# Optimization experiments

Measured on AMD Instinct MI355X. Metric: run time of the kernel, lower is better.

Reference implementation:

```python
import jax, jax.numpy as jnp
import numpy as np

NUM_HEADS = 8


def _nearest_idx(x, x_grid):
    # x: [b,n,dx]; x_grid: [b,H,W,dx] regular grid -> flat nearest cell index [b,n]
    b = x.shape[0]
    H, W = x_grid.shape[1], x_grid.shape[2]
    gf = x_grid.reshape(b, H * W, -1)
    lo = gf[:, :1]   # min corner [b,1,dx]
    hi = gf[:, -1:]  # max corner [b,1,dx]
    dims = jnp.asarray([H, W], dtype=x.dtype)
    t = (x - lo) / (hi - lo) * (dims - 1.0)
    idx = jnp.clip(jnp.round(t), 0.0, dims - 1.0).astype(jnp.int32)  # [b,n,2]
    return idx[..., 0] * W + idx[..., 1]


def _cumcount(idx):
    # per-batch cumulative count of each value, in order of appearance
    b, n = idx.shape
    order = jnp.argsort(idx, axis=1, stable=True)
    s = jnp.take_along_axis(idx, order, axis=1)
    ar = jnp.arange(n)
    new_run = jnp.concatenate([jnp.ones((b, 1), bool), s[:, 1:] != s[:, :-1]], axis=1)
    run_start = jax.lax.cummax(jnp.where(new_run, ar, 0), axis=1)
    cc_sorted = (ar - run_start).astype(jnp.int32)
    return jnp.zeros((b, n), jnp.int32).at[jnp.arange(b)[:, None], order].set(cc_sorted)


def _mhca(q_in, kv, mask, Wq, Wk, Wv, Wo):
    # q_in: [B,1,e]; kv: [B,K,e]; mask: [B,K] (True = attend)
    B, K, e = kv.shape
    dh = e // NUM_HEADS
    q = (q_in @ Wq).reshape(B, 1, NUM_HEADS, dh)
    k = (kv @ Wk).reshape(B, K, NUM_HEADS, dh)
    v = (kv @ Wv).reshape(B, K, NUM_HEADS, dh)
    scores = jnp.einsum('bqhd,bkhd->bhqk', q, k) / jnp.sqrt(jnp.asarray(dh, q.dtype))
    scores = jnp.where(mask[:, None, None, :], scores, jnp.finfo(scores.dtype).min)
    attn = jax.nn.softmax(scores, axis=-1)
    out = jnp.einsum('bhqk,bkhd->bqhd', attn, v).reshape(B, 1, e)
    return out @ Wo


def setup_inputs() -> dict:
    key = jax.random.key(0)
    ks = jax.random.split(key, 8)
    b, n, e, H, W = 8, 8192, 128, 64, 64
    x = jax.random.uniform(ks[0], (b, n, 2), jnp.float32)
    z = jax.random.normal(ks[1], (b, n, e), jnp.float32)
    g0 = jnp.linspace(0.0, 1.0, H)
    g1 = jnp.linspace(0.0, 1.0, W)
    mg = jnp.stack(jnp.meshgrid(g0, g1, indexing='ij'), axis=-1)  # [H,W,2]
    x_grid = jnp.broadcast_to(mg, (b, H, W, 2)).astype(jnp.float32)
    z_grid = jax.random.normal(ks[2], (b, H, W, e), jnp.float32)
    latent = jax.random.normal(ks[3], (e,), jnp.float32)
    scale = 1.0 / np.sqrt(e).astype(np.float32)
    Wq = jax.random.normal(ks[4], (e, e), jnp.float32) * scale
    Wk = jax.random.normal(ks[5], (e, e), jnp.float32) * scale
    Wv = jax.random.normal(ks[6], (e, e), jnp.float32) * scale
    Wo = jax.random.normal(ks[7], (e, e), jnp.float32) * scale
    return {"x": x, "z": z, "x_grid": x_grid, "z_grid": z_grid, "latent": latent,
            "Wq": Wq, "Wk": Wk, "Wv": Wv, "Wo": Wo, "max_patch": 20}


def reference(x, z, x_grid, z_grid, latent, Wq, Wk, Wv, Wo, max_patch):
    b, n, e = z.shape
    H, W = x_grid.shape[1], x_grid.shape[2]
    S = H * W
    nearest = _nearest_idx(x, x_grid)                    # [b,n]
    cc = _cumcount(nearest)                              # [b,n]
    bidx = jnp.broadcast_to(jnp.arange(b)[:, None], (b, n))
    valid = cc < max_patch
    slot = jnp.where(valid, cc, 0)
    # ragged scatter: pack each point's z into its grid cell's padded sequence
    joint = jnp.zeros((b, S, max_patch, e), z.dtype)
    joint = joint.at[bidx, nearest, slot].add(z * valid[..., None].astype(z.dtype))
    zg_flat = z_grid.reshape(b, S, e)
    joint = jnp.concatenate([joint, zg_flat[:, :, None, :]], axis=2)  # [b,S,P+1,e]
    counts = jnp.zeros((b, S), jnp.int32).at[bidx, nearest].add(1)
    mask = jnp.arange(max_patch + 1)[None, None, :] < jnp.minimum(counts, max_patch)[..., None]
    mask = mask.at[..., -1].set(True)  # grid token always attended
    joint = joint.reshape(b * S, max_patch + 1, e)
    mask = mask.reshape(b * S, max_patch + 1)
    q = jnp.broadcast_to(latent, (b * S, 1, e))          # z0_grid queries
    zg = _mhca(q, joint, mask, Wq, Wk, Wv, Wo)           # [b*S,1,e]
    zg = zg.reshape(b, H, W, e)
    return x_grid, zg
```

## Files before the change

kernel.cpp:

```cpp
#include <hip/hip_runtime.h>
#include <hip/hip_bf16.h>
#include <cstdint>
#include <cstddef>

#define S_CELLS 4096
#define NB      8
#define NPTS    8192
#define E       128
#define MAXP    20
#define NHEADS  8
#define NPT_ROWS (NB * NPTS)
#define NGR_ROWS (NB * S_CELLS)
#define NTOK     (NPT_ROWS + NGR_ROWS)


typedef __attribute__((ext_vector_type(8))) short bf16x8;
typedef __attribute__((ext_vector_type(4))) float f32x4;

__device__ __forceinline__ unsigned short f2bf_bits(float f) {
    unsigned u = __float_as_uint(f);
    unsigned rounded = u + 0x7FFFu + ((u >> 16) & 1u);
    return (unsigned short)(rounded >> 16);
}
__device__ __forceinline__ float bf2f(unsigned short u) {
    return __uint_as_float(((unsigned)u) << 16);
}

__global__ void k_points(const float* __restrict__ x,
                         const float* __restrict__ x_grid,
                         int* __restrict__ counts,
                         int* __restrict__ slots,
                         float* __restrict__ out_xgrid) {
    int i = blockIdx.x * blockDim.x + threadIdx.x;
    if (i >= NB * NPTS) return;
    out_xgrid[i] = x_grid[i];

    int b = i >> 13;
    float x0 = x[(size_t)i * 2 + 0];
    float x1 = x[(size_t)i * 2 + 1];
    int i0 = (int)rintf(x0 * 63.0f);
    int i1 = (int)rintf(x1 * 63.0f);
    i0 = min(max(i0, 0), 63);
    i1 = min(max(i1, 0), 63);
    int cell = b * S_CELLS + i0 * 64 + i1;
    int slot = atomicAdd(&counts[cell], 1);
    if (slot < MAXP) slots[cell * MAXP + slot] = i & (NPTS - 1);
}

__global__ void k_prep(const float* __restrict__ latent,
                       const float* __restrict__ Wq,
                       const float* __restrict__ Wk,
                       float* __restrict__ A) {
    __shared__ float lat[E];
    __shared__ float q[E];
    int j = threadIdx.x;
    lat[j] = latent[j];
    __syncthreads();
    float acc = 0.0f;
    for (int i = 0; i < E; ++i) acc += lat[i] * Wq[i * E + j];
    q[j] = acc;
    __syncthreads();
    for (int h = 0; h < NHEADS; ++h) {
        float a = 0.0f;
        #pragma unroll
        for (int d = 0; d < 16; ++d) a += Wk[j * E + h * 16 + d] * q[h * 16 + d];
        A[j * NHEADS + h] = a * 0.25f;
    }
}

__device__ __forceinline__ bf16x8 load_afrag(const float* __restrict__ X,
                                             int row, int kq, int q) {
    const float4* xr = (const float4*)(X + (size_t)row * E);
    float4 lo = xr[kq * 8 + q * 2];
    float4 hi = xr[kq * 8 + q * 2 + 1];
    bf16x8 f;
    f[0] = (short)f2bf_bits(lo.x);
    f[1] = (short)f2bf_bits(lo.y);
    f[2] = (short)f2bf_bits(lo.z);
    f[3] = (short)f2bf_bits(lo.w);
    f[4] = (short)f2bf_bits(hi.x);
    f[5] = (short)f2bf_bits(hi.y);
    f[6] = (short)f2bf_bits(hi.z);
    f[7] = (short)f2bf_bits(hi.w);
    return f;
}
__device__ __forceinline__ bf16x8 load_afrag(const unsigned short* __restrict__ X,
                                             int row, int kq, int q) {
    return *(const bf16x8*)(X + (size_t)row * E + kq * 32 + q * 8);
}

__device__ __forceinline__ void store_out(float* C, size_t idx, float v) { C[idx] = v; }
__device__ __forceinline__ void store_out(unsigned short* C, size_t idx, float v) {
    C[idx] = f2bf_bits(v);
}

template <typename InT, typename OutT, bool WITH_SC, int MT>
__global__ void __launch_bounds__(256)
k_gemm_mfma(const InT* __restrict__ X1, int n1blocks,
            const InT* __restrict__ X2,
            const float* __restrict__ W,
            const float* __restrict__ Aw,
            OutT* __restrict__ C,
            float* __restrict__ SC) {
    __shared__ unsigned short W_t[144][136];

    const int t = threadIdx.x;

    for (int idx = t; idx < E * E; idx += 256) {
        int k = idx >> 7, n = idx & 127;
        W_t[n][k] = f2bf_bits(W[idx]);
    }
    if (WITH_SC) {
        for (int idx = t; idx < E * NHEADS; idx += 256) {
            int k = idx >> 3, h = idx & 7;
            W_t[128 + h][k] = f2bf_bits(Aw[idx]);
        }
        for (int idx = t; idx < 8 * 136; idx += 256) {
            int rr = idx / 136, cc = idx - rr * 136;
            W_t[136 + rr][cc] = 0;
        }
    }
    __syncthreads();

    const int lane = t & 63;
    const int wv   = t >> 6;
    const int cn   = lane & 15;
    const int q    = lane >> 4;

    const int rows_per_block = 4 * MT * 16;
    const int grow0 = blockIdx.x * rows_per_block;
    const InT* Xsrc;
    int srow;
    if (blockIdx.x < n1blocks) { Xsrc = X1; srow = grow0; }
    else                       { Xsrc = X2; srow = grow0 - n1blocks * rows_per_block; }

    const int NT = WITH_SC ? 9 : 8;
    f32x4 acc[MT][9];
    #pragma unroll
    for (int mt = 0; mt < MT; ++mt)
        #pragma unroll
        for (int nt = 0; nt < 9; ++nt)
            acc[mt][nt] = f32x4{0.0f, 0.0f, 0.0f, 0.0f};

    #pragma unroll
    for (int kq = 0; kq < 4; ++kq) {
        bf16x8 a[MT];
        #pragma unroll
        for (int mt = 0; mt < MT; ++mt)
            a[mt] = load_afrag(Xsrc, srow + wv * (MT * 16) + mt * 16 + cn, kq, q);
        #pragma unroll
        for (int nt = 0; nt < NT; ++nt) {
            const bf16x8 b = *(const bf16x8*)&W_t[nt * 16 + cn][kq * 32 + q * 8];
            #pragma unroll
            for (int mt = 0; mt < MT; ++mt)
                acc[mt][nt] = __builtin_amdgcn_mfma_f32_16x16x32_bf16(
                    a[mt], b, acc[mt][nt], 0, 0, 0);
        }
    }

    #pragma unroll
    for (int mt = 0; mt < MT; ++mt) {
        const int rb = grow0 + wv * (MT * 16) + mt * 16 + q * 4;
        #pragma unroll
        for (int nt = 0; nt < 8; ++nt)
            #pragma unroll
            for (int r = 0; r < 4; ++r)
                store_out(C, (size_t)(rb + r) * E + nt * 16 + cn, acc[mt][nt][r]);
        if (WITH_SC && cn < 8) {
            #pragma unroll
            for (int r = 0; r < 4; ++r)
                SC[(size_t)(rb + r) * NHEADS + cn] = acc[mt][8][r];
        }
    }
}

__global__ void __launch_bounds__(256)
k_attn(const int* __restrict__ counts,
       const int* __restrict__ slots,
       const float* __restrict__ SC,
       const unsigned short* __restrict__ V,
       unsigned short* __restrict__ out) {
    const int wv   = threadIdx.x >> 6;
    const int lane = threadIdx.x & 63;
    const int cell = blockIdx.x * 4 + wv;
    const int b    = cell >> 12;
    const int cnt  = counts[cell];
    const int m    = min(cnt, MAXP);

    const int h1 = lane >> 4;
    const int h2 = 4 + h1;

    int sl = (lane < m) ? slots[cell * MAXP + lane] : 0;

    size_t r0 = (size_t)(NPT_ROWS + cell);
    float m1 = SC[r0 * NHEADS + h1];
    float m2 = SC[r0 * NHEADS + h2];
    float s1 = 1.0f, s2 = 1.0f;
    float o1 = bf2f(V[r0 * E + lane]);
    float o2 = bf2f(V[r0 * E + 64 + lane]);

    const int base = b * NPTS;

    for (int t0 = 0; t0 < m; t0 += 4) {
        float a1v[4], a2v[4], v1v[4], v2v[4];
        #pragma unroll
        for (int j = 0; j < 4; ++j) {
            int pt = __shfl(sl, t0 + j, 64);
            size_t r = (size_t)(base + pt);
            bool val = (t0 + j) < m;
            float sa1 = SC[r * NHEADS + h1];
            float sa2 = SC[r * NHEADS + h2];
            a1v[j] = val ? sa1 : -1e30f;
            a2v[j] = val ? sa2 : -1e30f;
            v1v[j] = bf2f(V[r * E + lane]);
            v2v[j] = bf2f(V[r * E + 64 + lane]);
        }
        #pragma unroll
        for (int j = 0; j < 4; ++j) {
            float nm1 = fmaxf(m1, a1v[j]);
            float e1  = __expf(a1v[j] - nm1);
            float al1 = __expf(m1 - nm1);
            s1 = s1 * al1 + e1;
            o1 = o1 * al1 + e1 * v1v[j];
            m1 = nm1;

            float nm2 = fmaxf(m2, a2v[j]);
            float e2  = __expf(a2v[j] - nm2);
            float al2 = __expf(m2 - nm2);
            s2 = s2 * al2 + e2;
            o2 = o2 * al2 + e2 * v2v[j];
            m2 = nm2;
        }
    }

    out[(size_t)cell * E + lane]      = f2bf_bits(o1 / s1);
    out[(size_t)cell * E + 64 + lane] = f2bf_bits(o2 / s2);
}

extern "C" void kernel_launch(void* const* d_in, const int* in_sizes, int n_in,
                              void* d_out, int out_size, void* d_ws, size_t ws_size,
                              hipStream_t stream) {
    const float* x      = (const float*)d_in[0];
    const float* z      = (const float*)d_in[1];
    const float* x_grid = (const float*)d_in[2];
    const float* z_grid = (const float*)d_in[3];
    const float* latent = (const float*)d_in[4];
    const float* Wq     = (const float*)d_in[5];
    const float* Wk     = (const float*)d_in[6];
    const float* Wv     = (const float*)d_in[7];
    const float* Wo     = (const float*)d_in[8];

    char* ws = (char*)d_ws;
    int*            counts = (int*)(ws + 0);
    int*            slots  = (int*)(ws + 131072);
    float*          A      = (float*)(ws + 2752512);
    float*          SC     = (float*)(ws + 2756608);
    unsigned short* V      = (unsigned short*)(ws + 5902336);
    unsigned short* outb   = (unsigned short*)(ws + 31068160);

    float* out_xgrid = (float*)d_out;
    float* zg        = (float*)d_out + NB * NPTS;

    (void)hipMemsetAsync(counts, 0, NB * S_CELLS * sizeof(int), stream);

    k_points<<<(NB * NPTS) / 256, 256, 0, stream>>>(x, x_grid, counts, slots, out_xgrid);
    k_prep<<<1, 128, 0, stream>>>(latent, Wq, Wk, A);

    k_gemm_mfma<float, unsigned short, true, 2><<<768, 256, 0, stream>>>(
        z, 512, z_grid, Wv, A, V, SC);

    k_attn<<<(NB * S_CELLS) / 4, 256, 0, stream>>>(counts, slots, SC, V, outb);

    k_gemm_mfma<unsigned short, float, false, 1><<<512, 256, 0, stream>>>(
        outb, 512, nullptr, Wo, nullptr, zg, nullptr);
}
```

Before: 149.9 us.

## Fuse attention with output projection and fold query prep into point binning

Merges the k_prep kernel into block 0 of k_points and fuses the attention kernel with the Wo projection GEMM. The attention result for each cell now stays in shared memory instead of making a global bf16 round trip, and two launches are removed. Attention is reorganised so each wave processes 16 cells sequentially with one head per 8 lanes, loading two channels per lane and prefetching the next cell's slots. Weight staging into LDS now uses coalesced 4-wide reads and vector stores. The trade-off is fewer waves in flight for the gather-heavy attention (512 blocks of 16 serial cells instead of 8192 blocks of one cell each), and every block must stage Wo into shared memory.

```diff
diff --git a/kernel.cpp b/kernel.cpp
--- a/kernel.cpp
+++ b/kernel.cpp
@@ -16,6 +16,7 @@
 
 typedef __attribute__((ext_vector_type(8))) short bf16x8;
 typedef __attribute__((ext_vector_type(4))) float f32x4;
+typedef __attribute__((ext_vector_type(4))) unsigned short us4;
 
 __device__ __forceinline__ unsigned short f2bf_bits(float f) {
     unsigned u = __float_as_uint(f);
@@ -26,13 +27,36 @@
     return __uint_as_float(((unsigned)u) << 16);
 }
 
-__global__ void k_points(const float* __restrict__ x,
-                         const float* __restrict__ x_grid,
-                         int* __restrict__ counts,
-                         int* __restrict__ slots,
-                         float* __restrict__ out_xgrid) {
-    int i = blockIdx.x * blockDim.x + threadIdx.x;
-    if (i >= NB * NPTS) return;
+__device__ __forceinline__ void stage_w_t(const float* __restrict__ W,
+                                          unsigned short (*__restrict__ W_t)[136],
+                                          int t) {
+    #pragma unroll
+    for (int it = 0; it < 16; ++it) {
+        int id = t + it * 256;
+        int n  = id & 127;
+        int kc = id >> 7;
+        float w0 = W[(size_t)(4 * kc + 0) * E + n];
+        float w1 = W[(size_t)(4 * kc + 1) * E + n];
+        float w2 = W[(size_t)(4 * kc + 2) * E + n];
+        float w3 = W[(size_t)(4 * kc + 3) * E + n];
+        us4 v;
+        v.x = f2bf_bits(w0); v.y = f2bf_bits(w1);
+        v.z = f2bf_bits(w2); v.w = f2bf_bits(w3);
+        *(us4*)&W_t[n][4 * kc] = v;
+    }
+}
+
+__global__ void __launch_bounds__(256)
+k_points(const float* __restrict__ x,
+         const float* __restrict__ x_grid,
+         const float* __restrict__ latent,
+         const float* __restrict__ Wq,
+         const float* __restrict__ Wk,
+         int* __restrict__ counts,
+         int* __restrict__ slots,
+         float* __restrict__ A,
+         float* __restrict__ out_xgrid) {
+    int i = blockIdx.x * 256 + threadIdx.x;
     out_xgrid[i] = x_grid[i];
 
     int b = i >> 13;
@@ -45,31 +69,30 @@
     int cell = b * S_CELLS + i0 * 64 + i1;
     int slot = atomicAdd(&counts[cell], 1);
     if (slot < MAXP) slots[cell * MAXP + slot] = i & (NPTS - 1);
-}
-
-__global__ void k_prep(const float* __restrict__ latent,
-                       const float* __restrict__ Wq,
-                       const float* __restrict__ Wk,
-                       float* __restrict__ A) {
-    __shared__ float lat[E];
-    __shared__ float q[E];
-    int j = threadIdx.x;
-    lat[j] = latent[j];
-    __syncthreads();
-    float acc = 0.0f;
-    for (int i = 0; i < E; ++i) acc += lat[i] * Wq[i * E + j];
-    q[j] = acc;
-    __syncthreads();
-    for (int h = 0; h < NHEADS; ++h) {
-        float a = 0.0f;
-        #pragma unroll
-        for (int d = 0; d < 16; ++d) a += Wk[j * E + h * 16 + d] * q[h * 16 + d];
-        A[j * NHEADS + h] = a * 0.25f;
-    }
-}
-
-__device__ __forceinline__ bf16x8 load_afrag(const float* __restrict__ X,
-                                             int row, int kq, int q) {
+
+    if (blockIdx.x == 0) {
+        __shared__ float lat[E];
+        __shared__ float qv[E];
+        const int t = threadIdx.x;
+        const int j = t & 127;
+        if (t < E) lat[t] = latent[t];
+        __syncthreads();
+        float acc = 0.0f;
+        for (int k2 = 0; k2 < E; ++k2) acc += lat[k2] * Wq[k2 * E + j];
+        qv[j] = acc;
+        __syncthreads();
+        const int hb = (t >> 7) * 4;
+        for (int h = hb; h < hb + 4; ++h) {
+            float a = 0.0f;
+            #pragma unroll
+            for (int d = 0; d < 16; ++d) a += Wk[j * E + h * 16 + d] * qv[h * 16 + d];
+            A[j * NHEADS + h] = a * 0.25f;
+        }
+    }
+}
+
+__device__ __forceinline__ bf16x8 load_afrag_f32(const float* __restrict__ X,
+                                                 int row, int kq, int q) {
     const float4* xr = (const float4*)(X + (size_t)row * E);
     float4 lo = xr[kq * 8 + q * 2];
     float4 hi = xr[kq * 8 + q * 2 + 1];
@@ -84,41 +107,25 @@
     f[7] = (short)f2bf_bits(hi.w);
     return f;
 }
-__device__ __forceinline__ bf16x8 load_afrag(const unsigned short* __restrict__ X,
-                                             int row, int kq, int q) {
-    return *(const bf16x8*)(X + (size_t)row * E + kq * 32 + q * 8);
-}
-
-__device__ __forceinline__ void store_out(float* C, size_t idx, float v) { C[idx] = v; }
-__device__ __forceinline__ void store_out(unsigned short* C, size_t idx, float v) {
-    C[idx] = f2bf_bits(v);
-}
-
-template <typename InT, typename OutT, bool WITH_SC, int MT>
+
 __global__ void __launch_bounds__(256)
-k_gemm_mfma(const InT* __restrict__ X1, int n1blocks,
-            const InT* __restrict__ X2,
-            const float* __restrict__ W,
-            const float* __restrict__ Aw,
-            OutT* __restrict__ C,
-            float* __restrict__ SC) {
+k_gemm1(const float* __restrict__ Xz,
+        const float* __restrict__ Xg,
+        const float* __restrict__ Wv,
+        const float* __restrict__ Aw,
+        unsigned short* __restrict__ V,
+        float* __restrict__ SC) {
     __shared__ unsigned short W_t[144][136];
 
     const int t = threadIdx.x;
-
-    for (int idx = t; idx < E * E; idx += 256) {
-        int k = idx >> 7, n = idx & 127;
-        W_t[n][k] = f2bf_bits(W[idx]);
-    }
-    if (WITH_SC) {
-        for (int idx = t; idx < E * NHEADS; idx += 256) {
-            int k = idx >> 3, h = idx & 7;
-            W_t[128 + h][k] = f2bf_bits(Aw[idx]);
-        }
-        for (int idx = t; idx < 8 * 136; idx += 256) {
-            int rr = idx / 136, cc = idx - rr * 136;
-            W_t[136 + rr][cc] = 0;
-        }
+    stage_w_t(Wv, W_t, t);
+    for (int idx = t; idx < E * NHEADS; idx += 256) {
+        int k = idx >> 3, hh = idx & 7;
+        W_t[128 + hh][k] = f2bf_bits(Aw[idx]);
+    }
+    for (int idx = t; idx < 8 * 136; idx += 256) {
+        int rr = idx / 136, cc = idx - rr * 136;
+        W_t[136 + rr][cc] = 0;
     }
     __syncthreads();
 
@@ -127,46 +134,44 @@
     const int cn   = lane & 15;
     const int q    = lane >> 4;
 
-    const int rows_per_block = 4 * MT * 16;
-    const int grow0 = blockIdx.x * rows_per_block;
-    const InT* Xsrc;
+    const int grow0 = blockIdx.x * 128;
+    const float* Xsrc;
     int srow;
-    if (blockIdx.x < n1blocks) { Xsrc = X1; srow = grow0; }
-    else                       { Xsrc = X2; srow = grow0 - n1blocks * rows_per_block; }
-
-    const int NT = WITH_SC ? 9 : 8;
-    f32x4 acc[MT][9];
-    #pragma unroll
-    for (int mt = 0; mt < MT; ++mt)
+    if (blockIdx.x < 512) { Xsrc = Xz; srow = grow0; }
+    else                  { Xsrc = Xg; srow = grow0 - 65536; }
+
+    f32x4 acc[2][9];
+    #pragma unroll
+    for (int mt = 0; mt < 2; ++mt)
         #pragma unroll
         for (int nt = 0; nt < 9; ++nt)
             acc[mt][nt] = f32x4{0.0f, 0.0f, 0.0f, 0.0f};
 
     #pragma unroll
     for (int kq = 0; kq < 4; ++kq) {
-        bf16x8 a[MT];
-        #pragma unroll
-        for (int mt = 0; mt < MT; ++mt)
-            a[mt] = load_afrag(Xsrc, srow + wv * (MT * 16) + mt * 16 + cn, kq, q);
-        #pragma unroll
-        for (int nt = 0; nt < NT; ++nt) {
+        bf16x8 a[2];
+        #pragma unroll
+        for (int mt = 0; mt < 2; ++mt)
+            a[mt] = load_afrag_f32(Xsrc, srow + wv * 32 + mt * 16 + cn, kq, q);
+        #pragma unroll
+        for (int nt = 0; nt < 9; ++nt) {
             const bf16x8 b = *(const bf16x8*)&W_t[nt * 16 + cn][kq * 32 + q * 8];
             #pragma unroll
-            for (int mt = 0; mt < MT; ++mt)
+            for (int mt = 0; mt < 2; ++mt)
                 acc[mt][nt] = __builtin_amdgcn_mfma_f32_16x16x32_bf16(
                     a[mt], b, acc[mt][nt], 0, 0, 0);
         }
     }
 
     #pragma unroll
-    for (int mt = 0; mt < MT; ++mt) {
-        const int rb = grow0 + wv * (MT * 16) + mt * 16 + q * 4;
+    for (int mt = 0; mt < 2; ++mt) {
+        const int rb = grow0 + wv * 32 + mt * 16 + q * 4;
         #pragma unroll
         for (int nt = 0; nt < 8; ++nt)
             #pragma unroll
             for (int r = 0; r < 4; ++r)
-                store_out(C, (size_t)(rb + r) * E + nt * 16 + cn, acc[mt][nt][r]);
-        if (WITH_SC && cn < 8) {
+                V[(size_t)(rb + r) * E + nt * 16 + cn] = f2bf_bits(acc[mt][nt][r]);
+        if (cn < 8) {
             #pragma unroll
             for (int r = 0; r < 4; ++r)
                 SC[(size_t)(rb + r) * NHEADS + cn] = acc[mt][8][r];
@@ -175,66 +180,97 @@
 }
 
 __global__ void __launch_bounds__(256)
-k_attn(const int* __restrict__ counts,
-       const int* __restrict__ slots,
-       const float* __restrict__ SC,
-       const unsigned short* __restrict__ V,
-       unsigned short* __restrict__ out) {
-    const int wv   = threadIdx.x >> 6;
-    const int lane = threadIdx.x & 63;
-    const int cell = blockIdx.x * 4 + wv;
-    const int b    = cell >> 12;
-    const int cnt  = counts[cell];
-    const int m    = min(cnt, MAXP);
-
-    const int h1 = lane >> 4;
-    const int h2 = 4 + h1;
-
-    int sl = (lane < m) ? slots[cell * MAXP + lane] : 0;
-
-    size_t r0 = (size_t)(NPT_ROWS + cell);
-    float m1 = SC[r0 * NHEADS + h1];
-    float m2 = SC[r0 * NHEADS + h2];
-    float s1 = 1.0f, s2 = 1.0f;
-    float o1 = bf2f(V[r0 * E + lane]);
-    float o2 = bf2f(V[r0 * E + 64 + lane]);
-
+k_attn_proj(const int* __restrict__ counts,
+            const int* __restrict__ slots,
+            const float* __restrict__ SC,
+            const unsigned short* __restrict__ V,
+            const float* __restrict__ Wo,
+            float* __restrict__ zg) {
+    __shared__ unsigned short W_t[128][136];
+    __shared__ unsigned short X_s[64][136];
+
+    const int t = threadIdx.x;
+    stage_w_t(Wo, W_t, t);
+
+    const int lane = t & 63;
+    const int wv   = t >> 6;
+    const int cell_base = blockIdx.x * 64 + wv * 16;
+    const int b    = blockIdx.x >> 6;
     const int base = b * NPTS;
-
-    for (int t0 = 0; t0 < m; t0 += 4) {
-        float a1v[4], a2v[4], v1v[4], v2v[4];
-        #pragma unroll
-        for (int j = 0; j < 4; ++j) {
-            int pt = __shfl(sl, t0 + j, 64);
-            size_t r = (size_t)(base + pt);
-            bool val = (t0 + j) < m;
-            float sa1 = SC[r * NHEADS + h1];
-            float sa2 = SC[r * NHEADS + h2];
-            a1v[j] = val ? sa1 : -1e30f;
-            a2v[j] = val ? sa2 : -1e30f;
-            v1v[j] = bf2f(V[r * E + lane]);
-            v2v[j] = bf2f(V[r * E + 64 + lane]);
-        }
-        #pragma unroll
-        for (int j = 0; j < 4; ++j) {
-            float nm1 = fmaxf(m1, a1v[j]);
-            float e1  = __expf(a1v[j] - nm1);
-            float al1 = __expf(m1 - nm1);
-            s1 = s1 * al1 + e1;
-            o1 = o1 * al1 + e1 * v1v[j];
-            m1 = nm1;
-
-            float nm2 = fmaxf(m2, a2v[j]);
-            float e2  = __expf(a2v[j] - nm2);
-            float al2 = __expf(m2 - nm2);
-            s2 = s2 * al2 + e2;
-            o2 = o2 * al2 + e2 * v2v[j];
-            m2 = nm2;
-        }
-    }
-
-    out[(size_t)cell * E + lane]      = f2bf_bits(o1 / s1);
-    out[(size_t)cell * E + 64 + lane] = f2bf_bits(o2 / s2);
+    const int h    = lane >> 3;
+
+    int cnt_all = (lane < 16) ? counts[cell_base + lane] : 0;
+    int slw     = (lane < MAXP) ? slots[(size_t)cell_base * MAXP + lane] : 0;
+
+    for (int ci = 0; ci < 16; ++ci) {
+        const int cell = cell_base + ci;
+        const int m = min(__shfl(cnt_all, ci, 64), MAXP);
+        int slw_n = 0;
+        if (ci < 15)
+            slw_n = (lane < MAXP) ? slots[(size_t)(cell + 1) * MAXP + lane] : 0;
+
+        size_t r0 = (size_t)(NPT_ROWS + cell);
+        float mm = SC[r0 * NHEADS + h];
+        float ss = 1.0f;
+        unsigned v0 = *(const unsigned*)(V + r0 * E + 2 * lane);
+        float o0 = bf2f((unsigned short)v0);
+        float o1 = bf2f((unsigned short)(v0 >> 16));
+
+        for (int t0 = 0; t0 < m; t0 += 4) {
+            float av[4], p0[4], p1[4];
+            #pragma unroll
+            for (int j = 0; j < 4; ++j) {
+                int pt = __shfl(slw, t0 + j, 64);
+                bool val = (t0 + j) < m;
+                pt = val ? pt : 0;
+                size_t r = (size_t)(base + pt);
+                float sa = SC[r * NHEADS + h];
+                av[j] = val ? sa : -1e30f;
+                unsigned vv = *(const unsigned*)(V + r * E + 2 * lane);
+                p0[j] = bf2f((unsigned short)vv);
+                p1[j] = bf2f((unsigned short)(vv >> 16));
+            }
+            #pragma unroll
+            for (int j = 0; j < 4; ++j) {
+                float nm = fmaxf(mm, av[j]);
+                float e  = __expf(av[j] - nm);
+                float al = __expf(mm - nm);
+                ss = ss * al + e;
+                o0 = o0 * al + e * p0[j];
+                o1 = o1 * al + e * p1[j];
+                mm = nm;
+            }
+        }
+        float inv = 1.0f / ss;
+        unsigned packed = (unsigned)f2bf_bits(o0 * inv)
+                        | ((unsigned)f2bf_bits(o1 * inv) << 16);
+        *(unsigned*)&X_s[wv * 16 + ci][2 * lane] = packed;
+        slw = slw_n;
+    }
+    __syncthreads();
+
+    const int cn = lane & 15;
+    const int q  = lane >> 4;
+    f32x4 acc[8];
+    #pragma unroll
+    for (int nt = 0; nt < 8; ++nt) acc[nt] = f32x4{0.0f, 0.0f, 0.0f, 0.0f};
+
+    #pragma unroll
+    for (int kq = 0; kq < 4; ++kq) {
+        bf16x8 a = *(const bf16x8*)&X_s[wv * 16 + cn][kq * 32 + q * 8];
+        #pragma unroll
+        for (int nt = 0; nt < 8; ++nt) {
+            const bf16x8 bb = *(const bf16x8*)&W_t[nt * 16 + cn][kq * 32 + q * 8];
+            acc[nt] = __builtin_amdgcn_mfma_f32_16x16x32_bf16(a, bb, acc[nt], 0, 0, 0);
+        }
+    }
+
+    const int rb = blockIdx.x * 64 + wv * 16 + q * 4;
+    #pragma unroll
+    for (int nt = 0; nt < 8; ++nt)
+        #pragma unroll
+        for (int r = 0; r < 4; ++r)
+            zg[(size_t)(rb + r) * E + nt * 16 + cn] = acc[nt][r];
 }
 
 extern "C" void kernel_launch(void* const* d_in, const int* in_sizes, int n_in,
@@ -256,21 +292,16 @@
     float*          A      = (float*)(ws + 2752512);
     float*          SC     = (float*)(ws + 2756608);
     unsigned short* V      = (unsigned short*)(ws + 5902336);
-    unsigned short* outb   = (unsigned short*)(ws + 31068160);
 
     float* out_xgrid = (float*)d_out;
     float* zg        = (float*)d_out + NB * NPTS;
 
     (void)hipMemsetAsync(counts, 0, NB * S_CELLS * sizeof(int), stream);
 
-    k_points<<<(NB * NPTS) / 256, 256, 0, stream>>>(x, x_grid, counts, slots, out_xgrid);
-    k_prep<<<1, 128, 0, stream>>>(latent, Wq, Wk, A);
-
-    k_gemm_mfma<float, unsigned short, true, 2><<<768, 256, 0, stream>>>(
-        z, 512, z_grid, Wv, A, V, SC);
-
-    k_attn<<<(NB * S_CELLS) / 4, 256, 0, stream>>>(counts, slots, SC, V, outb);
-
-    k_gemm_mfma<unsigned short, float, false, 1><<<512, 256, 0, stream>>>(
-        outb, 512, nullptr, Wo, nullptr, zg, nullptr);
-}
+    k_points<<<256, 256, 0, stream>>>(x, x_grid, latent, Wq, Wk,
+                                      counts, slots, A, out_xgrid);
+
+    k_gemm1<<<768, 256, 0, stream>>>(z, z_grid, Wv, A, V, SC);
+
+    k_attn_proj<<<512, 256, 0, stream>>>(counts, slots, SC, V, Wo, zg);
+}
```

Result: no change. 148.4 us (-1.0%).
